# Optimization experiments

Measured on AMD Instinct MI355X. Metric: run time of the kernel, lower is better.

Reference implementation:

```python
import jax, jax.numpy as jnp
import numpy as np

N_HEAD = 16
NEG_INF = -1e30  # finite mask value, safe for softmax/grad


def setup_inputs() -> dict:
    key = jax.random.key(0)
    k1, k2, k3 = jax.random.split(key, 3)
    B, T, C = 4, 2049, 1024
    x = jax.random.normal(k1, (B, T, C), dtype=jnp.float32)
    W_attn = jax.random.normal(k2, (C, 3 * C), dtype=jnp.float32) * (1.0 / np.sqrt(C))
    W_proj = jax.random.normal(k3, (C, C), dtype=jnp.float32) * (1.0 / np.sqrt(C))
    return {"x": x, "W_attn": W_attn, "W_proj": W_proj}


def reference(x, W_attn, W_proj):
    B, T, C = x.shape
    H = N_HEAD
    D = C // H
    qkv = x @ W_attn                                  # (B, T, 3C)
    q, k, v = jnp.split(qkv, 3, axis=-1)
    q = q.reshape(B, T, H, D).transpose(0, 2, 1, 3)   # (B, H, T, D)
    k = k.reshape(B, T, H, D).transpose(0, 2, 1, 3)
    v = v.reshape(B, T, H, D).transpose(0, 2, 1, 3)
    # hybrid mask: causal tril, but state token (row 0) attends to ALL positions
    mask = jnp.tril(jnp.ones((T, T), dtype=bool))
    mask = mask.at[0, :].set(True)
    scale = 1.0 / np.sqrt(D)
    scores = jnp.einsum('bhtd,bhsd->bhts', q, k) * scale
    scores = jnp.where(mask[None, None, :, :], scores, NEG_INF)
    att = jax.nn.softmax(scores, axis=-1)
    y = jnp.einsum('bhts,bhsd->bhtd', att, v)         # (B, H, T, D)
    y = y.transpose(0, 2, 1, 3).reshape(B, T, C)
    return y @ W_proj
```

## Files before the change

### kernel.cpp

```cpp
#include <hip/hip_runtime.h>

typedef __attribute__((ext_vector_type(8))) __bf16 bf16x8;
typedef __attribute__((ext_vector_type(4))) __bf16 bf16x4;
typedef __attribute__((ext_vector_type(4))) float f32x4;

#define GLDS(g, l) __builtin_amdgcn_global_load_lds( \
    (__attribute__((address_space(1))) void*)(void*)(g), \
    (__attribute__((address_space(3))) void*)(void*)(l), 16, 0, 0)

constexpr int T_REAL = 2049;
constexpr int Tp     = 2112;
constexpr int Mreal  = 8196;
constexpr int Mp     = 8320;
constexpr int GK     = 1024;

constexpr float QSCALE = 0.125f * 1.4426950408889634f;

__global__ __launch_bounds__(256) void cvt_x(const float* __restrict__ x,
                                             __bf16* __restrict__ xb) {
    size_t i = ((size_t)blockIdx.x * 256 + threadIdx.x) * 4;
    float4 v = make_float4(0.f, 0.f, 0.f, 0.f);
    if (i < (size_t)Mreal * GK) v = *(const float4*)(x + i);
    bf16x4 o;
    o.x = (__bf16)v.x; o.y = (__bf16)v.y; o.z = (__bf16)v.z; o.w = (__bf16)v.w;
    *(bf16x4*)(xb + i) = o;
}

__global__ __launch_bounds__(256) void transpose_w(const float* __restrict__ W,
                                                   __bf16* __restrict__ Wt,
                                                   int K, int N) {
    __shared__ float tile[64][65];
    const int n0 = blockIdx.x * 64, k0 = blockIdx.y * 64;
    const int tx = threadIdx.x & 63, ty = threadIdx.x >> 6;
#pragma unroll
    for (int j = 0; j < 16; j++) {
        int rk = ty + j * 4;
        tile[rk][tx] = W[(size_t)(k0 + rk) * N + n0 + tx];
    }
    __syncthreads();
#pragma unroll
    for (int j = 0; j < 16; j++) {
        int rn = ty + j * 4;
        Wt[(size_t)(n0 + rn) * K + k0 + tx] = (__bf16)tile[tx][rn];
    }
}

__global__ __launch_bounds__(256) void transpose_v(const __bf16* __restrict__ v,
                                                   __bf16* __restrict__ vT) {
    __shared__ __bf16 tl[64][72];
    const int bh = blockIdx.y, t0 = blockIdx.x * 64;
    const int tid = threadIdx.x;
    const __bf16* src = v + ((size_t)bh * Tp + t0) * 64;
    {
        const int r = tid >> 3, c = (tid & 7) * 8;
        *(bf16x8*)&tl[r][c]      = *(const bf16x8*)(src + r * 64 + c);
        *(bf16x8*)&tl[r + 32][c] = *(const bf16x8*)(src + (r + 32) * 64 + c);
    }
    __syncthreads();
    __bf16* dst = vT + (size_t)bh * 64 * Tp + t0;
    {
        const int d = tid >> 3, tc = (tid & 7) * 8;
        bf16x8 a, b;
#pragma unroll
        for (int i = 0; i < 8; i++) {
            a[i] = tl[tc + i][d];
            b[i] = tl[tc + i][d + 32];
        }
        *(bf16x8*)(dst + (size_t)d * Tp + tc)        = a;
        *(bf16x8*)(dst + (size_t)(d + 32) * Tp + tc) = b;
    }
}

template <int EPI>
__global__ __launch_bounds__(256)
void gemm128(const __bf16* __restrict__ A, const __bf16* __restrict__ Bt,
             float* __restrict__ outp,
             __bf16* __restrict__ qout, __bf16* __restrict__ kout,
             __bf16* __restrict__ vout) {
    __shared__ __bf16 As[128 * 64];
    __shared__ __bf16 Bs[128 * 64];

    const int tid = threadIdx.x, lane = tid & 63, w = tid >> 6;
    const int wr = w >> 1, wc = w & 1;
    const int quad = lane >> 4, l15 = lane & 15, l7 = l15 & 7;
    const int m0 = blockIdx.y * 128, n0 = blockIdx.x * 128;

    const int row0 = w * 32 + (lane >> 3);
    const int gc8 = ((lane & 7) ^ ((lane >> 3) & 7)) * 8;
    const __bf16* agp = A + (size_t)(m0 + row0) * GK + gc8;
    const __bf16* bgp = Bt + (size_t)(n0 + row0) * GK + gc8;
    __bf16* lap = &As[(w * 256 + lane) * 8];
    __bf16* lbp = &Bs[(w * 256 + lane) * 8];

    f32x4 acc[4][4] = {};

    for (int k0 = 0; k0 < GK; k0 += 64) {
#pragma unroll
        for (int s = 0; s < 4; s++) {
            GLDS(agp + (size_t)s * 8 * GK + k0, lap + s * 512);
            GLDS(bgp + (size_t)s * 8 * GK + k0, lbp + s * 512);
        }
        __syncthreads();
#pragma unroll
        for (int kk = 0; kk < 2; kk++) {
            bf16x8 fa[4], fb[4];
#pragma unroll
            for (int i = 0; i < 4; i++)
                fa[i] = *(const bf16x8*)&As[(wr * 64 + i * 16 + l15) * 64 + (((kk * 4 + quad) ^ l7) * 8)];
#pragma unroll
            for (int j = 0; j < 4; j++)
                fb[j] = *(const bf16x8*)&Bs[(wc * 64 + j * 16 + l15) * 64 + (((kk * 4 + quad) ^ l7) * 8)];
#pragma unroll
            for (int i = 0; i < 4; i++)
#pragma unroll
                for (int j = 0; j < 4; j++)
                    acc[i][j] = __builtin_amdgcn_mfma_f32_16x16x32_bf16(fa[i], fb[j], acc[i][j], 0, 0, 0);
        }
        __syncthreads();
    }

    if constexpr (EPI == 0) {
        const int which = n0 >> 10;
        const int h = ((n0 + wc * 64) >> 6) & 15;
        __bf16* op = (which == 0) ? qout : (which == 1) ? kout : vout;
        const float scl = (which == 0) ? QSCALE : 1.0f;
        __bf16* wls = &As[w * 2048];
#pragma unroll
        for (int p = 0; p < 2; p++) {
            if (p) __syncthreads();
#pragma unroll
            for (int i2 = 0; i2 < 2; i2++)
#pragma unroll
                for (int j = 0; j < 4; j++)
#pragma unroll
                    for (int r = 0; r < 4; r++) {
                        const int lrow = i2 * 16 + quad * 4 + r;
                        const int cX = (j * 2 + (l15 >> 3)) ^ (lrow & 7);
                        wls[lrow * 64 + cX * 8 + (l15 & 7)] =
                            (__bf16)(acc[p * 2 + i2][j][r] * scl);
                    }
            __syncthreads();
#pragma unroll
            for (int it = 0; it < 4; it++) {
                const int lrow = (lane >> 3) + it * 8;
                bf16x8 vv = *(const bf16x8*)&wls[lrow * 64 + (((lane & 7) ^ (lrow & 7)) * 8)];
                const int m = m0 + wr * 64 + p * 32 + lrow;
                if (m < Mreal) {
                    const int b = m / T_REAL;
                    const int t = m - b * T_REAL;
                    *(bf16x8*)&op[(((size_t)(b * 16 + h)) * Tp + t) * 64 + (lane & 7) * 8] = vv;
                }
            }
        }
    } else {
        float* wlf = (float*)&As[0] + w * 1024;
#pragma unroll
        for (int p = 0; p < 4; p++) {
            if (p) __syncthreads();
#pragma unroll
            for (int j = 0; j < 4; j++)
#pragma unroll
                for (int r = 0; r < 4; r++) {
                    const int lrow = quad * 4 + r;
                    const int cX = (j * 4 + (l15 >> 2)) ^ (lrow & 7);
                    wlf[lrow * 64 + cX * 4 + (l15 & 3)] = acc[p][j][r];
                }
            __syncthreads();
#pragma unroll
            for (int it = 0; it < 4; it++) {
                const int lrow = lane >> 2;
                const int c = (lane & 3) + it * 4;
                f32x4 vv = *(const f32x4*)&wlf[lrow * 64 + ((c ^ (lrow & 7)) * 4)];
                const int m = m0 + wr * 64 + p * 16 + lrow;
                if (m < Mreal)
                    *(f32x4*)&outp[(size_t)m * 1024 + n0 + wc * 64 + c * 4] = vv;
            }
        }
    }
}

__global__ __launch_bounds__(512, 6)
void attn(const __bf16* __restrict__ q, const __bf16* __restrict__ kk,
          const __bf16* __restrict__ vT, __bf16* __restrict__ y) {
    __shared__ __bf16 Ks[2][64 * 64];
    __shared__ __bf16 Vs[2][64 * 64];
    __shared__ __bf16 Pq[8][16 * 64];

    static const int QA[17] = {0,31,29,27,25,23,21,19,17,15,13,11,9,7,5,3,1};
    static const int QB[17] = {32,30,28,26,24,22,20,18,16,14,12,10,8,6,4,2,-1};

    const int tid = threadIdx.x, lane = tid & 63, w = tid >> 6;
    const int quad = lane >> 4, l15 = lane & 15;
    const int l7 = l15 & 7;
    const int z = blockIdx.x;
    const int slot = z >> 6;
    const int zz = z & 63;
    const int bh = (zz & 7) * 8 + (zz >> 3);

    const int qtA = QA[slot];
    const int qt = (w < 4) ? qtA : QB[slot];
    const bool active = qt >= 0;
    const int qts = active ? qt : 0;
    const int q0 = qts * 64;
    const int qg = q0 + (w & 3) * 16 + l15;
    const int myNt = (qts == 0) ? 32 : qts;
    const int ntmaxB = (qtA == 0) ? 32 : qtA;

    const __bf16* kgb = kk + (size_t)bh * Tp * 64;
    const __bf16* vgb = vT + (size_t)bh * 64 * Tp;
    const int b = bh >> 4, h = bh & 15;

    const int r0 = tid >> 3;
    const int s0 = ((tid & 7) ^ (r0 & 7)) * 8;
    const int koff = r0 * 64 + s0;
    const int voff = r0 * Tp + s0;

    bf16x8 qa0, qa1;
    {
        const __bf16* qp = q + ((size_t)bh * Tp + qg) * 64 + quad * 8;
        qa0 = *(const bf16x8*)qp;
        qa1 = *(const bf16x8*)(qp + 32);
    }

    f32x4 o[4] = {};
    float mrow = -3e38f, lrow = 0.f;

    GLDS(kgb + koff, &Ks[0][tid * 8]);
    GLDS(vgb + voff, &Vs[0][tid * 8]);

    int cur = 0;
    for (int nt = 0; nt <= ntmaxB; ++nt) {
        __syncthreads();
        if (nt < ntmaxB) {
            GLDS(kgb + (size_t)(nt + 1) * 4096 + koff, &Ks[cur ^ 1][tid * 8]);
            GLDS(vgb + (size_t)(nt + 1) * 64 + voff, &Vs[cur ^ 1][tid * 8]);
        }
        if (active && nt <= myNt) {
            const int kv0 = nt * 64;

            f32x4 st[4];
#pragma unroll
            for (int j = 0; j < 4; j++) {
                const __bf16* krow = &Ks[cur][(j * 16 + l15) * 64];
                bf16x8 klo = *(const bf16x8*)(krow + ((quad ^ l7) * 8));
                bf16x8 khi = *(const bf16x8*)(krow + (((quad + 4) ^ l7) * 8));
                f32x4 zzv = {0.f, 0.f, 0.f, 0.f};
                zzv = __builtin_amdgcn_mfma_f32_16x16x32_bf16(klo, qa0, zzv, 0, 0, 0);
                st[j] = __builtin_amdgcn_mfma_f32_16x16x32_bf16(khi, qa1, zzv, 0, 0, 0);
            }

            if (nt >= qts) {
#pragma unroll
                for (int j = 0; j < 4; j++)
#pragma unroll
                    for (int r = 0; r < 4; r++) {
                        const int kvg = kv0 + j * 16 + quad * 4 + r;
                        const bool valid = (kvg <= qg) || (qg == 0 && kvg < T_REAL);
                        st[j][r] = valid ? st[j][r] : -1e30f;
                    }
            }

            float mx = -3e38f;
#pragma unroll
            for (int j = 0; j < 4; j++)
#pragma unroll
                for (int r = 0; r < 4; r++) mx = fmaxf(mx, st[j][r]);
            mx = fmaxf(mx, __shfl_xor(mx, 16));
            mx = fmaxf(mx, __shfl_xor(mx, 32));
            const float mn = fmaxf(mrow, mx);
            const float alpha = __builtin_amdgcn_exp2f(mrow - mn);
            mrow = mn;

            float rs = 0.f;
            bf16x4 pk[4];
#pragma unroll
            for (int j = 0; j < 4; j++) {
                float p0 = __builtin_amdgcn_exp2f(st[j][0] - mn);
                float p1 = __builtin_amdgcn_exp2f(st[j][1] - mn);
                float p2 = __builtin_amdgcn_exp2f(st[j][2] - mn);
                float p3 = __builtin_amdgcn_exp2f(st[j][3] - mn);
                rs += (p0 + p1) + (p2 + p3);
                pk[j].x = (__bf16)p0; pk[j].y = (__bf16)p1;
                pk[j].z = (__bf16)p2; pk[j].w = (__bf16)p3;
            }
            rs += __shfl_xor(rs, 16);
            rs += __shfl_xor(rs, 32);
            lrow = lrow * alpha + rs;
#pragma unroll
            for (int nf = 0; nf < 4; nf++)
#pragma unroll
                for (int r = 0; r < 4; r++) o[nf][r] *= alpha;

#pragma unroll
            for (int j = 0; j < 4; j++)
                *(bf16x4*)&Pq[w][l15 * 64 + (((2 * j + (quad >> 1)) ^ l7) * 8) + (quad & 1) * 4] = pk[j];

#pragma unroll
            for (int kc = 0; kc < 2; kc++) {
                bf16x8 pb = *(const bf16x8*)&Pq[w][l15 * 64 + (((kc * 4 + quad) ^ l7) * 8)];
#pragma unroll
                for (int nf = 0; nf < 4; nf++) {
                    bf16x8 va = *(const bf16x8*)&Vs[cur][(nf * 16 + l15) * 64 + (((kc * 4 + quad) ^ l7) * 8)];
                    o[nf] = __builtin_amdgcn_mfma_f32_16x16x32_bf16(va, pb, o[nf], 0, 0, 0);
                }
            }
        }
        cur ^= 1;
    }

    if (active && qg < T_REAL) {
        const float inv = 1.0f / lrow;
        __bf16* yp = y + ((size_t)(b * T_REAL + qg)) * 1024 + h * 64 + quad * 4;
#pragma unroll
        for (int nf = 0; nf < 4; nf++) {
            bf16x4 pko;
            pko.x = (__bf16)(o[nf][0] * inv);
            pko.y = (__bf16)(o[nf][1] * inv);
            pko.z = (__bf16)(o[nf][2] * inv);
            pko.w = (__bf16)(o[nf][3] * inv);
            *(bf16x4*)(yp + nf * 16) = pko;
        }
    }
}

extern "C" void kernel_launch(void* const* d_in, const int* in_sizes, int n_in,
                              void* d_out, int out_size, void* d_ws, size_t ws_size,
                              hipStream_t stream) {
    const float* x  = (const float*)d_in[0];
    const float* Wa = (const float*)d_in[1];
    const float* Wp = (const float*)d_in[2];
    float* out = (float*)d_out;

    char* ws = (char*)d_ws;
    constexpr size_t SZ_XB  = (size_t)Mp * GK * 2;
    constexpr size_t SZ_WAT = (size_t)3072 * GK * 2;
    constexpr size_t SZ_WPT = (size_t)1024 * GK * 2;
    constexpr size_t SZ_QK  = (size_t)64 * Tp * 64 * 2;
    __bf16* xb   = (__bf16*)(ws);
    __bf16* WaT  = (__bf16*)(ws + SZ_XB);
    __bf16* WpT  = (__bf16*)(ws + SZ_XB + SZ_WAT);
    __bf16* qb   = (__bf16*)(ws + SZ_XB + SZ_WAT + SZ_WPT);
    __bf16* kb   = (__bf16*)(ws + SZ_XB + SZ_WAT + SZ_WPT + SZ_QK);
    __bf16* vTb  = (__bf16*)(ws + SZ_XB + SZ_WAT + SZ_WPT + 2 * SZ_QK);
    __bf16* shrd = (__bf16*)(ws + SZ_XB + SZ_WAT + SZ_WPT + 3 * SZ_QK);
    __bf16* vpre = shrd;
    __bf16* yb   = shrd;

    cvt_x<<<(Mp * GK) / 1024, 256, 0, stream>>>(x, xb);
    transpose_w<<<dim3(48, 16), 256, 0, stream>>>(Wa, WaT, 1024, 3072);
    transpose_w<<<dim3(16, 16), 256, 0, stream>>>(Wp, WpT, 1024, 1024);

    gemm128<0><<<dim3(24, 65), 256, 0, stream>>>(xb, WaT, nullptr, qb, kb, vpre);
    transpose_v<<<dim3(33, 64), 256, 0, stream>>>(vpre, vTb);
    attn<<<1088, 512, 0, stream>>>(qb, kb, vTb, yb);
    gemm128<1><<<dim3(8, 65), 256, 0, stream>>>(yb, WpT, out, nullptr, nullptr, nullptr);
}
```

Before: 285.8 us.

## Replace QKV projection GEMM with 256x256-tile double-buffered 8-wave kernel

Adds a new gemm256 kernel for the QKV projection. It uses 256x256 output tiles, 512 threads and double-buffered LDS staging through global_load_lds. The K loop is split into four MFMA phases, interleaved with prefetches and raised wave priority. The larger tile raises arithmetic intensity and cuts redundant global loads compared with the 128x128 kernel. In exchange it uses 128KB of LDS and many accumulator registers per block, pads M further to 8448, and launches far fewer blocks (396), which may leave the device less well balanced.

```diff
diff --git a/kernel.cpp b/kernel.cpp
--- a/kernel.cpp
+++ b/kernel.cpp
@@ -11,7 +11,7 @@
 constexpr int T_REAL = 2049;
 constexpr int Tp     = 2112;
 constexpr int Mreal  = 8196;
-constexpr int Mp     = 8320;
+constexpr int Mp     = 8448;
 constexpr int GK     = 1024;
 
 constexpr float QSCALE = 0.125f * 1.4426950408889634f;
@@ -68,6 +68,164 @@
         }
         *(bf16x8*)(dst + (size_t)d * Tp + tc)        = a;
         *(bf16x8*)(dst + (size_t)(d + 32) * Tp + tc) = b;
+    }
+}
+
+__global__ __launch_bounds__(512)
+void gemm256(const __bf16* __restrict__ A, const __bf16* __restrict__ Bt,
+             __bf16* __restrict__ qout, __bf16* __restrict__ kout,
+             __bf16* __restrict__ vout) {
+    __shared__ __align__(16) __bf16 As[2][16384];
+    __shared__ __align__(16) __bf16 Bs[2][16384];
+
+    const int tid = threadIdx.x, lane = tid & 63, w = tid >> 6;
+    const int wr = w >> 2, wc = w & 3;
+    const int quad = lane >> 4, l15 = lane & 15, l7 = l15 & 7;
+    const int m0 = blockIdx.y * 256, n0 = blockIdx.x * 256;
+
+    const int sr = tid >> 3;
+    const int sc = ((tid & 7) ^ (sr & 7)) * 8;
+    const __bf16* ag = A  + (size_t)(m0 + sr) * GK + sc;
+    const __bf16* bg = Bt + (size_t)(n0 + sr) * GK + sc;
+    const int ldst = tid * 8;
+
+#define STG_A(T, h) do { const __bf16* s_ = ag + (size_t)(h) * 128 * GK + (T) * 64; \
+    GLDS(s_, &As[(T) & 1][(h) * 8192 + ldst]); \
+    GLDS(s_ + (size_t)64 * GK, &As[(T) & 1][(h) * 8192 + 4096 + ldst]); } while (0)
+#define STG_B(T, h) do { const __bf16* s_ = bg + (size_t)(h) * 128 * GK + (T) * 64; \
+    GLDS(s_, &Bs[(T) & 1][(h) * 8192 + ldst]); \
+    GLDS(s_ + (size_t)64 * GK, &Bs[(T) & 1][(h) * 8192 + 4096 + ldst]); } while (0)
+
+    f32x4 acc[8][4] = {};
+    bf16x8 a[8], b0[4], b1[4];
+
+    STG_A(0, 0); STG_B(0, 1); STG_A(0, 1); STG_B(0, 0); STG_A(1, 0); STG_B(1, 1);
+    asm volatile("s_waitcnt vmcnt(4)" ::: "memory");
+    __builtin_amdgcn_s_barrier();
+
+    constexpr int NT = GK / 64;
+
+#pragma unroll 1
+    for (int T = 0; T < NT; ++T) {
+        const int p = T & 1;
+
+#pragma unroll
+        for (int f = 0; f < 4; ++f) {
+            const int R = f * 32 + wr * 16 + l15;
+            a[f * 2 + 0] = *(const bf16x8*)&As[p][R * 64 + ((quad ^ l7) * 8)];
+            a[f * 2 + 1] = *(const bf16x8*)&As[p][R * 64 + (((4 + quad) ^ l7) * 8)];
+        }
+#pragma unroll
+        for (int n = 0; n < 2; ++n) {
+            const int R = n * 64 + wc * 16 + l15;
+            b0[n * 2 + 0] = *(const bf16x8*)&Bs[p][R * 64 + ((quad ^ l7) * 8)];
+            b0[n * 2 + 1] = *(const bf16x8*)&Bs[p][R * 64 + (((4 + quad) ^ l7) * 8)];
+        }
+        if (T + 1 < NT) { STG_A(T + 1, 1); STG_B(T + 1, 0); }
+        __builtin_amdgcn_s_barrier();
+        asm volatile("s_waitcnt lgkmcnt(0)" ::: "memory");
+        __builtin_amdgcn_sched_barrier(0);
+        __builtin_amdgcn_s_setprio(1);
+#pragma unroll
+        for (int f = 0; f < 4; ++f)
+#pragma unroll
+            for (int n = 0; n < 2; ++n) {
+                acc[f][n] = __builtin_amdgcn_mfma_f32_16x16x32_bf16(a[f*2+0], b0[n*2+0], acc[f][n], 0, 0, 0);
+                acc[f][n] = __builtin_amdgcn_mfma_f32_16x16x32_bf16(a[f*2+1], b0[n*2+1], acc[f][n], 0, 0, 0);
+            }
+        __builtin_amdgcn_s_setprio(0);
+        __builtin_amdgcn_s_barrier();
+
+#pragma unroll
+        for (int n = 0; n < 2; ++n) {
+            const int R = 128 + n * 64 + wc * 16 + l15;
+            b1[n * 2 + 0] = *(const bf16x8*)&Bs[p][R * 64 + ((quad ^ l7) * 8)];
+            b1[n * 2 + 1] = *(const bf16x8*)&Bs[p][R * 64 + (((4 + quad) ^ l7) * 8)];
+        }
+        __builtin_amdgcn_s_barrier();
+        asm volatile("s_waitcnt lgkmcnt(0)" ::: "memory");
+        __builtin_amdgcn_sched_barrier(0);
+        __builtin_amdgcn_s_setprio(1);
+#pragma unroll
+        for (int f = 0; f < 4; ++f)
+#pragma unroll
+            for (int n = 0; n < 2; ++n) {
+                acc[f][2+n] = __builtin_amdgcn_mfma_f32_16x16x32_bf16(a[f*2+0], b1[n*2+0], acc[f][2+n], 0, 0, 0);
+                acc[f][2+n] = __builtin_amdgcn_mfma_f32_16x16x32_bf16(a[f*2+1], b1[n*2+1], acc[f][2+n], 0, 0, 0);
+            }
+        __builtin_amdgcn_s_setprio(0);
+        __builtin_amdgcn_s_barrier();
+
+#pragma unroll
+        for (int f = 0; f < 4; ++f) {
+            const int R = 128 + f * 32 + wr * 16 + l15;
+            a[f * 2 + 0] = *(const bf16x8*)&As[p][R * 64 + ((quad ^ l7) * 8)];
+            a[f * 2 + 1] = *(const bf16x8*)&As[p][R * 64 + (((4 + quad) ^ l7) * 8)];
+        }
+        if (T + 2 < NT) STG_A(T + 2, 0);
+        __builtin_amdgcn_s_barrier();
+        asm volatile("s_waitcnt lgkmcnt(0)" ::: "memory");
+        __builtin_amdgcn_sched_barrier(0);
+        __builtin_amdgcn_s_setprio(1);
+#pragma unroll
+        for (int f = 0; f < 4; ++f)
+#pragma unroll
+            for (int n = 0; n < 2; ++n) {
+                acc[4+f][2+n] = __builtin_amdgcn_mfma_f32_16x16x32_bf16(a[f*2+0], b1[n*2+0], acc[4+f][2+n], 0, 0, 0);
+                acc[4+f][2+n] = __builtin_amdgcn_mfma_f32_16x16x32_bf16(a[f*2+1], b1[n*2+1], acc[4+f][2+n], 0, 0, 0);
+            }
+        __builtin_amdgcn_s_setprio(0);
+        __builtin_amdgcn_s_barrier();
+
+        if (T + 2 < NT) STG_B(T + 2, 1);
+        __builtin_amdgcn_s_barrier();
+        asm volatile("s_waitcnt lgkmcnt(0)" ::: "memory");
+        __builtin_amdgcn_sched_barrier(0);
+        __builtin_amdgcn_s_setprio(1);
+#pragma unroll
+        for (int f = 0; f < 4; ++f)
+#pragma unroll
+            for (int n = 0; n < 2; ++n) {
+                acc[4+f][n] = __builtin_amdgcn_mfma_f32_16x16x32_bf16(a[f*2+0], b0[n*2+0], acc[4+f][n], 0, 0, 0);
+                acc[4+f][n] = __builtin_amdgcn_mfma_f32_16x16x32_bf16(a[f*2+1], b0[n*2+1], acc[4+f][n], 0, 0, 0);
+            }
+        __builtin_amdgcn_s_setprio(0);
+        if (T < NT - 2) { asm volatile("s_waitcnt vmcnt(4)" ::: "memory"); }
+        else            { asm volatile("s_waitcnt vmcnt(0)" ::: "memory"); }
+        __builtin_amdgcn_s_barrier();
+    }
+#undef STG_A
+#undef STG_B
+
+    const int which = n0 >> 10;
+    __bf16* op = (which == 0) ? qout : (which == 1) ? kout : vout;
+    const float scl = (which == 0) ? QSCALE : 1.0f;
+    __bf16* ep = &As[0][0];
+    const int rr = tid >> 4, cc = tid & 15;
+#pragma unroll
+    for (int f = 0; f < 8; ++f) {
+        __syncthreads();
+#pragma unroll
+        for (int n = 0; n < 4; ++n) {
+            const int col = (n & 1) * 64 + wc * 16 + (n >> 1) * 128 + l15;
+#pragma unroll
+            for (int r = 0; r < 4; ++r)
+                ep[(wr * 16 + quad * 4 + r) * 264 + col] = (__bf16)(acc[f][n][r] * scl);
+        }
+        __syncthreads();
+        const int m = m0 + (f & 3) * 32 + (f >> 2) * 128 + rr;
+        if (m < Mreal) {
+            const int b = m / T_REAL;
+            const int t = m - b * T_REAL;
+#pragma unroll
+            for (int g = 0; g < 2; ++g) {
+                const int c8 = (cc + g * 16) * 8;
+                bf16x8 vv = *(const bf16x8*)&ep[rr * 264 + c8];
+                const int gc = n0 + c8;
+                const int h = (gc >> 6) & 15;
+                *(bf16x8*)&op[((size_t)(b * 16 + h) * Tp + t) * 64 + (gc & 63)] = vv;
+            }
+        }
     }
 }
 
@@ -350,7 +508,7 @@
     transpose_w<<<dim3(48, 16), 256, 0, stream>>>(Wa, WaT, 1024, 3072);
     transpose_w<<<dim3(16, 16), 256, 0, stream>>>(Wp, WpT, 1024, 1024);
 
-    gemm128<0><<<dim3(24, 65), 256, 0, stream>>>(xb, WaT, nullptr, qb, kb, vpre);
+    gemm256<<<dim3(12, 33), 512, 0, stream>>>(xb, WaT, qb, kb, vpre);
     transpose_v<<<dim3(33, 64), 256, 0, stream>>>(vpre, vTb);
     attn<<<1088, 512, 0, stream>>>(qb, kb, vTb, yb);
     gemm128<1><<<dim3(8, 65), 256, 0, stream>>>(yb, WpT, out, nullptr, nullptr, nullptr);
```

New measurement: 278.2 us. -2.7%, faster.
